# Performance work log

Hardware: AMD Instinct MI355X
Metric: run time of the kernel (lower is better)

Reference implementation:

```python
import jax, jax.numpy as jnp
import numpy as np

N, E, NNZ, F = 65536, 16384, 786432, 128
ALPHA, BETA = 0.5, 0.5


def _linear(x, w, b):
    # torch nn.Linear: x @ W^T + b, W is [out,in]
    return x @ w.T + b


def _spmm_to_edges(vals, node_idx, hedge_idx, m):
    # (sparse [E,N]) @ m[N,F] -> [E,F]
    return jax.ops.segment_sum(vals[:, None] * m[node_idx], hedge_idx, num_segments=E)


def _spmm_to_nodes(vals, node_idx, hedge_idx, m):
    # (sparse [N,E]) @ m[E,F] -> [N,F]
    return jax.ops.segment_sum(vals[:, None] * m[hedge_idx], node_idx, num_segments=N)


def setup_inputs() -> dict:
    key = jax.random.key(0)
    ks = jax.random.split(key, 16)
    stdv = 1.0 / np.sqrt(F)
    u = lambda k, shp: jax.random.uniform(k, shp, jnp.float32, -stdv, stdv)
    return {
        "x": jax.random.normal(ks[0], (N, F), jnp.float32),
        "y": jax.random.normal(ks[1], (E, F), jnp.float32),
        "node_idx": jax.random.randint(ks[2], (NNZ,), 0, N, jnp.int32),
        "hedge_idx": jax.random.randint(ks[3], (NNZ,), 0, E, jnp.int32),
        "hd_vals": jax.random.uniform(ks[4], (NNZ,), jnp.float32),
        "hb_vals": jax.random.uniform(ks[5], (NNZ,), jnp.float32),
        "dhwd_vals": jax.random.uniform(ks[6], (NNZ,), jnp.float32),
        "bhub_vals": jax.random.uniform(ks[7], (NNZ,), jnp.float32),
        "Qv_w": u(ks[8], (F, F)), "Qv_b": u(ks[9], (F,)),
        "Qe_w": u(ks[10], (F, F)), "Qe_b": u(ks[11], (F,)),
        "Pe_w": u(ks[12], (F, F)), "Pe_b": u(ks[13], (F,)),
        "Pv_w": u(ks[14], (F, F)), "Pv_b": u(ks[15], (F,)),
    }


def reference(x, y, node_idx, hedge_idx, hd_vals, hb_vals, dhwd_vals, bhub_vals,
              Qv_w, Qv_b, Qe_w, Qe_b, Pe_w, Pe_b, Pv_w, Pv_b):
    qvx = _linear(x, Qv_w, Qv_b)          # [N,F]
    qey = _linear(y, Qe_w, Qe_b)          # [E,F]
    pey = _linear(y, Pe_w, Pe_b)          # [E,F]
    pvx = _linear(x, Pv_w, Pv_b)          # [N,F]
    # X = DHWD @ (alpha * (HD @ Qv(x)) + (1-alpha) * Qe(y))
    t_e = ALPHA * _spmm_to_edges(hd_vals, node_idx, hedge_idx, qvx) + (1.0 - ALPHA) * qey
    X = _spmm_to_nodes(dhwd_vals, node_idx, hedge_idx, t_e)
    # Y = BHUB @ (beta * (HB @ Pe(y)) + (1-beta) * Pv(x))
    t_n = BETA * _spmm_to_nodes(hb_vals, node_idx, hedge_idx, pey) + (1.0 - BETA) * pvx
    Y = _spmm_to_edges(bhub_vals, node_idx, hedge_idx, t_n)
    return (X, Y)
```

## Files before the change

kernel.cpp:

```cpp
#include <hip/hip_runtime.h>

#define F 128
#define NN 65536
#define EE 16384
#define NNZT 786432

typedef __attribute__((ext_vector_type(8))) short bfrag8;
typedef __attribute__((ext_vector_type(4))) float f32x4;

__device__ __forceinline__ unsigned int bfrn(float f) {
    unsigned int u = __float_as_uint(f);
    return (u + 0x7fffu + ((u >> 16) & 1u)) >> 16;
}

__global__ void hist_kernel(const int4* __restrict__ hedge_idx4,
                            const int4* __restrict__ node_idx4,
                            int* __restrict__ cnt_e, int* __restrict__ cnt_n) {
    int i = blockIdx.x * 256 + threadIdx.x;
    int4 e = hedge_idx4[i];
    int4 n = node_idx4[i];
    atomicAdd(&cnt_e[e.x], 1);
    atomicAdd(&cnt_e[e.y], 1);
    atomicAdd(&cnt_e[e.z], 1);
    atomicAdd(&cnt_e[e.w], 1);
    atomicAdd(&cnt_n[n.x], 1);
    atomicAdd(&cnt_n[n.y], 1);
    atomicAdd(&cnt_n[n.z], 1);
    atomicAdd(&cnt_n[n.w], 1);
}

__global__ __launch_bounds__(1024) void scan_p1(const int* __restrict__ cnt,
                                                int* __restrict__ ofs,
                                                int* __restrict__ bsum) {
    __shared__ int wsum[16];
    int t = threadIdx.x, lane = t & 63, w = t >> 6;
    int g = blockIdx.x * 1024 + t;
    int v = cnt[g];
    int inc = v;
#pragma unroll
    for (int d = 1; d < 64; d <<= 1) {
        int u = __shfl_up(inc, d);
        if (lane >= d) inc += u;
    }
    if (lane == 63) wsum[w] = inc;
    __syncthreads();
    if (t < 16) {
        int s = wsum[t];
#pragma unroll
        for (int d = 1; d < 16; d <<= 1) {
            int u = __shfl_up(s, d);
            if (t >= d) s += u;
        }
        wsum[t] = s;
    }
    __syncthreads();
    int woff = (w == 0) ? 0 : wsum[w - 1];
    ofs[g] = woff + inc - v;
    if (t == 1023) bsum[blockIdx.x] = wsum[15];
}

__global__ void scan_p2(int* __restrict__ bsum, int nb, int* __restrict__ ofs_end) {
    int lane = threadIdx.x;
    int v = (lane < nb) ? bsum[lane] : 0;
    int inc = v;
#pragma unroll
    for (int d = 1; d < 64; d <<= 1) {
        int u = __shfl_up(inc, d);
        if (lane >= d) inc += u;
    }
    if (lane < nb) bsum[lane] = inc - v;
    if (lane == 63) *ofs_end = inc;
}

__global__ __launch_bounds__(1024) void scan_p3(int* __restrict__ ofs,
                                                const int* __restrict__ bsum) {
    int g = blockIdx.x * 1024 + threadIdx.x;
    ofs[g] += bsum[blockIdx.x];
}

__global__ void fill_kernel(const int* __restrict__ node_idx, const int* __restrict__ hedge_idx,
                            const float* __restrict__ hd_vals, const float* __restrict__ hb_vals,
                            const float* __restrict__ dhwd_vals, const float* __restrict__ bhub_vals,
                            const int* __restrict__ ofs_e, const int* __restrict__ ofs_n,
                            int* __restrict__ cur_e, int* __restrict__ cur_n,
                            int* __restrict__ csr_e_node, float* __restrict__ csr_e_v1, float* __restrict__ csr_e_v2,
                            int* __restrict__ csr_n_edge, float* __restrict__ csr_n_v1, float* __restrict__ csr_n_v2) {
    int i = blockIdx.x * 256 + threadIdx.x;
    int e = hedge_idx[i];
    int n = node_idx[i];
    int pe = atomicAdd(&cur_e[e], 1);
    int oe = ofs_e[e] + pe;
    csr_e_node[oe] = n;
    csr_e_v1[oe] = 0.5f * hd_vals[i];
    csr_e_v2[oe] = bhub_vals[i];
    int pn = atomicAdd(&cur_n[n], 1);
    int on = ofs_n[n] + pn;
    csr_n_edge[on] = e;
    csr_n_v1[on] = 0.5f * hb_vals[i];
    csr_n_v2[on] = dhwd_vals[i];
}

__global__ void wprep_kernel(const float* __restrict__ W0, const float* __restrict__ W1,
                             const float* __restrict__ W2, const float* __restrict__ W3,
                             unsigned short* __restrict__ whi, unsigned short* __restrict__ wlo) {
    int mat = blockIdx.x >> 6;
    int off = (blockIdx.x & 63) * 256 + threadIdx.x;
    const float* W = (mat == 0) ? W0 : (mat == 1) ? W1 : (mat == 2) ? W2 : W3;
    float f = W[off];
    unsigned int h = bfrn(f);
    float hf = __uint_as_float(h << 16);
    unsigned int l = bfrn(f - hf);
    int idx = mat * 16384 + off;
    whi[idx] = (unsigned short)h;
    wlo[idx] = (unsigned short)l;
}

__global__ __launch_bounds__(256, 2) void gemm_mfma(const float* __restrict__ in,
                                                    const unsigned short* __restrict__ whi,
                                                    const unsigned short* __restrict__ wlo,
                                                    const float* __restrict__ bA,
                                                    const float* __restrict__ bB,
                                                    float* __restrict__ outA,
                                                    float* __restrict__ outB) {
    __shared__ uint4 AH[2][4][64];
    __shared__ uint4 AL[2][4][64];
    int t = threadIdx.x;
    int wv = t >> 6, lane = t & 63;
    int row0 = blockIdx.x * 128;

    int mat = wv >> 1;
    const unsigned short* wh = whi + mat * 16384;
    const unsigned short* wl = wlo + mat * 16384;
    int colbase = (wv & 1) * 64;
    int ln15 = lane & 15;
    int kb = 8 * (lane >> 4);

    bfrag8 bh[4][4], bl[4][4];
#pragma unroll
    for (int ct = 0; ct < 4; ++ct) {
        int n = colbase + ct * 16 + ln15;
#pragma unroll
        for (int ks = 0; ks < 4; ++ks) {
            bh[ct][ks] = *(const bfrag8*)&wh[n * 128 + ks * 32 + kb];
            bl[ct][ks] = *(const bfrag8*)&wl[n * 128 + ks * 32 + kb];
        }
    }
    const float* bias = mat ? bB : bA;
    float biasv[4];
#pragma unroll
    for (int ct = 0; ct < 4; ++ct) biasv[ct] = bias[colbase + ct * 16 + ln15];
    float* outp = mat ? outB : outA;

    auto STAGE = [&](int rt, int b) {
        int r = row0 + rt * 16 + ln15;
        int k0 = wv * 32 + kb;
        const float* p = &in[(size_t)r * 128 + k0];
        float4 f0 = *(const float4*)p;
        float4 f1 = *(const float4*)(p + 4);
        float fs[8] = {f0.x, f0.y, f0.z, f0.w, f1.x, f1.y, f1.z, f1.w};
        unsigned int hi[4], lo[4];
#pragma unroll
        for (int q = 0; q < 4; ++q) {
            unsigned int h0 = bfrn(fs[2 * q]);
            unsigned int h1 = bfrn(fs[2 * q + 1]);
            float hf0 = __uint_as_float(h0 << 16);
            float hf1 = __uint_as_float(h1 << 16);
            unsigned int l0 = bfrn(fs[2 * q] - hf0);
            unsigned int l1 = bfrn(fs[2 * q + 1] - hf1);
            hi[q] = h0 | (h1 << 16);
            lo[q] = l0 | (l1 << 16);
        }
        AH[b][wv][lane] = make_uint4(hi[0], hi[1], hi[2], hi[3]);
        AL[b][wv][lane] = make_uint4(lo[0], lo[1], lo[2], lo[3]);
    };

    STAGE(0, 0);
    __syncthreads();
    for (int rt = 0; rt < 8; ++rt) {
        int b = rt & 1;
        if (rt < 7) STAGE(rt + 1, b ^ 1);
        f32x4 acc[4];
#pragma unroll
        for (int ct = 0; ct < 4; ++ct) acc[ct] = (f32x4){0.f, 0.f, 0.f, 0.f};
#pragma unroll
        for (int ks = 0; ks < 4; ++ks) {
            bfrag8 ah = *(const bfrag8*)&AH[b][ks][lane];
            bfrag8 al = *(const bfrag8*)&AL[b][ks][lane];
#pragma unroll
            for (int ct = 0; ct < 4; ++ct)
                acc[ct] = __builtin_amdgcn_mfma_f32_16x16x32_bf16(ah, bh[ct][ks], acc[ct], 0, 0, 0);
#pragma unroll
            for (int ct = 0; ct < 4; ++ct)
                acc[ct] = __builtin_amdgcn_mfma_f32_16x16x32_bf16(ah, bl[ct][ks], acc[ct], 0, 0, 0);
#pragma unroll
            for (int ct = 0; ct < 4; ++ct)
                acc[ct] = __builtin_amdgcn_mfma_f32_16x16x32_bf16(al, bh[ct][ks], acc[ct], 0, 0, 0);
        }
        int rbase = row0 + rt * 16 + (lane >> 4) * 4;
#pragma unroll
        for (int ct = 0; ct < 4; ++ct) {
            int c = colbase + ct * 16 + ln15;
#pragma unroll
            for (int rg = 0; rg < 4; ++rg)
                outp[(size_t)(rbase + rg) * 128 + c] = acc[ct][rg] + biasv[ct];
        }
        __syncthreads();
    }
}

template <int U, bool NT>
__global__ __launch_bounds__(256) void spmm_gather4(const int* __restrict__ ofs,
                                                    const int* __restrict__ tgt,
                                                    const float* __restrict__ val,
                                                    const float* __restrict__ src,
                                                    float* __restrict__ out,
                                                    float init_scale) {
    int row = blockIdx.x * 4 + (threadIdx.x >> 6);
    int lane = threadIdx.x & 63;
    int half = lane >> 5;
    int li = lane & 31;
    int o0 = ofs[row], o1 = ofs[row + 1];
    float4 acc = {0.f, 0.f, 0.f, 0.f};
    int j = o0;
    for (; j + 2 * U - 1 < o1; j += 2 * U) {
        int tg[U];
        float v[U];
#pragma unroll
        for (int u = 0; u < U; ++u) {
            tg[u] = tgt[j + 2 * u + half];
            v[u] = val[j + 2 * u + half];
        }
        float4 m[U];
#pragma unroll
        for (int u = 0; u < U; ++u) m[u] = *(const float4*)&src[(size_t)tg[u] * F + li * 4];
#pragma unroll
        for (int u = 0; u < U; ++u) {
            acc.x += v[u] * m[u].x;
            acc.y += v[u] * m[u].y;
            acc.z += v[u] * m[u].z;
            acc.w += v[u] * m[u].w;
        }
    }
    for (; j < o1; j += 2) {
        int idx = j + half;
        bool ok = idx < o1;
        int tg = ok ? tgt[idx] : tgt[o0];
        float v = ok ? val[idx] : 0.f;
        float4 m = *(const float4*)&src[(size_t)tg * F + li * 4];
        acc.x += v * m.x;
        acc.y += v * m.y;
        acc.z += v * m.z;
        acc.w += v * m.w;
    }
    acc.x += __shfl_down(acc.x, 32);
    acc.y += __shfl_down(acc.y, 32);
    acc.z += __shfl_down(acc.z, 32);
    acc.w += __shfl_down(acc.w, 32);
    if (half == 0) {
        float4* op = (float4*)&out[(size_t)row * F + li * 4];
        if (init_scale != 0.0f) {
            float4 in0 = *op;
            acc.x += init_scale * in0.x;
            acc.y += init_scale * in0.y;
            acc.z += init_scale * in0.z;
            acc.w += init_scale * in0.w;
        }
        if (NT) {
            __builtin_nontemporal_store(*(f32x4*)&acc, (f32x4*)op);
        } else {
            *op = acc;
        }
    }
}

extern "C" void kernel_launch(void* const* d_in, const int* in_sizes, int n_in,
                              void* d_out, int out_size, void* d_ws, size_t ws_size,
                              hipStream_t stream) {
    const float* x = (const float*)d_in[0];
    const float* y = (const float*)d_in[1];
    const int* node_idx = (const int*)d_in[2];
    const int* hedge_idx = (const int*)d_in[3];
    const float* hd_vals = (const float*)d_in[4];
    const float* hb_vals = (const float*)d_in[5];
    const float* dhwd_vals = (const float*)d_in[6];
    const float* bhub_vals = (const float*)d_in[7];
    const float* Qv_w = (const float*)d_in[8];
    const float* Qv_b = (const float*)d_in[9];
    const float* Qe_w = (const float*)d_in[10];
    const float* Qe_b = (const float*)d_in[11];
    const float* Pe_w = (const float*)d_in[12];
    const float* Pe_b = (const float*)d_in[13];
    const float* Pv_w = (const float*)d_in[14];
    const float* Pv_b = (const float*)d_in[15];

    float* X = (float*)d_out;
    float* Y = (float*)d_out + (size_t)NN * F;
    float* qvx = X;
    float* pey = Y;

    char* w = (char*)d_ws;
    float* t_n        = (float*)(w + 0);
    float* t_e        = (float*)(w + 33554432);
    int*   csr_e_node = (int*)  (w + 41943040);
    float* csr_e_v1   = (float*)(w + 45088768);
    float* csr_e_v2   = (float*)(w + 48234496);
    int*   csr_n_edge = (int*)  (w + 51380224);
    float* csr_n_v1   = (float*)(w + 54525952);
    float* csr_n_v2   = (float*)(w + 57671680);
    int*   cnt_e      = (int*)  (w + 60817408);
    int*   cnt_n      = (int*)  (w + 60882944);
    int*   cur_e      = (int*)  (w + 61145088);
    int*   cur_n      = (int*)  (w + 61210624);
    int*   ofs_e      = (int*)  (w + 61472768);
    int*   ofs_n      = (int*)  (w + 61538560);
    int*   bsum       = (int*)  (w + 61800960);
    unsigned short* whi = (unsigned short*)(w + 60882944);
    unsigned short* wlo = (unsigned short*)(w + 60882944 + 131072);

    (void)hipMemsetAsync(cnt_e, 0, (size_t)2 * (EE + NN) * 4, stream);

    hist_kernel<<<NNZT / 1024, 256, 0, stream>>>((const int4*)hedge_idx, (const int4*)node_idx,
                                                 cnt_e, cnt_n);

    scan_p1<<<EE / 1024, 1024, 0, stream>>>(cnt_e, ofs_e, bsum);
    scan_p2<<<1, 64, 0, stream>>>(bsum, EE / 1024, &ofs_e[EE]);
    scan_p3<<<EE / 1024, 1024, 0, stream>>>(ofs_e, bsum);
    scan_p1<<<NN / 1024, 1024, 0, stream>>>(cnt_n, ofs_n, bsum);
    scan_p2<<<1, 64, 0, stream>>>(bsum, NN / 1024, &ofs_n[NN]);
    scan_p3<<<NN / 1024, 1024, 0, stream>>>(ofs_n, bsum);

    fill_kernel<<<NNZT / 256, 256, 0, stream>>>(node_idx, hedge_idx, hd_vals, hb_vals,
                                                dhwd_vals, bhub_vals, ofs_e, ofs_n,
                                                cur_e, cur_n,
                                                csr_e_node, csr_e_v1, csr_e_v2,
                                                csr_n_edge, csr_n_v1, csr_n_v2);

    wprep_kernel<<<256, 256, 0, stream>>>(Qv_w, Pv_w, Qe_w, Pe_w, whi, wlo);

    gemm_mfma<<<NN / 128, 256, 0, stream>>>(x, whi, wlo, Qv_b, Pv_b, qvx, t_n);
    gemm_mfma<<<EE / 128, 256, 0, stream>>>(y, whi + 2 * 16384, wlo + 2 * 16384,
                                            Qe_b, Pe_b, t_e, pey);

    spmm_gather4<4, false><<<EE / 4, 256, 0, stream>>>(ofs_e, csr_e_node, csr_e_v1, qvx, t_e, 0.5f);
    spmm_gather4<4, false><<<NN / 4, 256, 0, stream>>>(ofs_n, csr_n_edge, csr_n_v1, pey, t_n, 0.5f);

    spmm_gather4<4, true><<<NN / 4, 256, 0, stream>>>(ofs_n, csr_n_edge, csr_n_v2, t_e, X, 0.0f);
    spmm_gather4<4, true><<<EE / 4, 256, 0, stream>>>(ofs_e, csr_e_node, csr_e_v2, t_n, Y, 0.0f);
}
```

Baseline: 555.9 us.

## Store gathered intermediates in bf16 and replace CSR value copies with inverse permutation

The GEMM outputs and the intermediate t_e/t_n that get gathered by the SpMMs are now stored as bf16, which halves the bytes of each random row gather. The fill kernel now writes only an inverse permutation instead of copying indices and four value arrays into CSR order. The SpMMs look up the index and value through that permutation, and each quarter-wave gathers 16-byte bf16 row chunks. This trades numerical precision in the intermediates (bf16 rounding) and an extra level of indirect loads for less fill-kernel traffic and less gather bandwidth.

```diff
diff --git a/kernel.cpp b/kernel.cpp
--- a/kernel.cpp
+++ b/kernel.cpp
@@ -78,26 +78,17 @@
     ofs[g] += bsum[blockIdx.x];
 }
 
-__global__ void fill_kernel(const int* __restrict__ node_idx, const int* __restrict__ hedge_idx,
-                            const float* __restrict__ hd_vals, const float* __restrict__ hb_vals,
-                            const float* __restrict__ dhwd_vals, const float* __restrict__ bhub_vals,
-                            const int* __restrict__ ofs_e, const int* __restrict__ ofs_n,
-                            int* __restrict__ cur_e, int* __restrict__ cur_n,
-                            int* __restrict__ csr_e_node, float* __restrict__ csr_e_v1, float* __restrict__ csr_e_v2,
-                            int* __restrict__ csr_n_edge, float* __restrict__ csr_n_v1, float* __restrict__ csr_n_v2) {
+__global__ void invfill_kernel(const int* __restrict__ node_idx, const int* __restrict__ hedge_idx,
+                               const int* __restrict__ ofs_e, const int* __restrict__ ofs_n,
+                               int* __restrict__ cur_e, int* __restrict__ cur_n,
+                               int* __restrict__ inv_e, int* __restrict__ inv_n) {
     int i = blockIdx.x * 256 + threadIdx.x;
     int e = hedge_idx[i];
+    int pe = atomicAdd(&cur_e[e], 1);
+    inv_e[ofs_e[e] + pe] = i;
     int n = node_idx[i];
-    int pe = atomicAdd(&cur_e[e], 1);
-    int oe = ofs_e[e] + pe;
-    csr_e_node[oe] = n;
-    csr_e_v1[oe] = 0.5f * hd_vals[i];
-    csr_e_v2[oe] = bhub_vals[i];
     int pn = atomicAdd(&cur_n[n], 1);
-    int on = ofs_n[n] + pn;
-    csr_n_edge[on] = e;
-    csr_n_v1[on] = 0.5f * hb_vals[i];
-    csr_n_v2[on] = dhwd_vals[i];
+    inv_n[ofs_n[n] + pn] = i;
 }
 
 __global__ void wprep_kernel(const float* __restrict__ W0, const float* __restrict__ W1,
@@ -115,13 +106,14 @@
     wlo[idx] = (unsigned short)l;
 }
 
+template <bool ABF16, bool BBF16>
 __global__ __launch_bounds__(256, 2) void gemm_mfma(const float* __restrict__ in,
                                                     const unsigned short* __restrict__ whi,
                                                     const unsigned short* __restrict__ wlo,
                                                     const float* __restrict__ bA,
                                                     const float* __restrict__ bB,
-                                                    float* __restrict__ outA,
-                                                    float* __restrict__ outB) {
+                                                    void* __restrict__ outA,
+                                                    void* __restrict__ outB) {
     __shared__ uint4 AH[2][4][64];
     __shared__ uint4 AL[2][4][64];
     int t = threadIdx.x;
@@ -149,7 +141,8 @@
     float biasv[4];
 #pragma unroll
     for (int ct = 0; ct < 4; ++ct) biasv[ct] = bias[colbase + ct * 16 + ln15];
-    float* outp = mat ? outB : outA;
+    void* outp = mat ? outB : outA;
+    bool obf = mat ? BBF16 : ABF16;
 
     auto STAGE = [&](int rt, int b) {
         int r = row0 + rt * 16 + ln15;
@@ -201,74 +194,87 @@
         for (int ct = 0; ct < 4; ++ct) {
             int c = colbase + ct * 16 + ln15;
 #pragma unroll
-            for (int rg = 0; rg < 4; ++rg)
-                outp[(size_t)(rbase + rg) * 128 + c] = acc[ct][rg] + biasv[ct];
+            for (int rg = 0; rg < 4; ++rg) {
+                float v = acc[ct][rg] + biasv[ct];
+                if (obf)
+                    ((unsigned short*)outp)[(size_t)(rbase + rg) * 128 + c] = (unsigned short)bfrn(v);
+                else
+                    ((float*)outp)[(size_t)(rbase + rg) * 128 + c] = v;
+            }
         }
         __syncthreads();
     }
 }
 
-template <int U, bool NT>
-__global__ __launch_bounds__(256) void spmm_gather4(const int* __restrict__ ofs,
-                                                    const int* __restrict__ tgt,
-                                                    const float* __restrict__ val,
-                                                    const float* __restrict__ src,
-                                                    float* __restrict__ out,
-                                                    float init_scale) {
+template <int U, bool BF16OUT, bool HASINIT>
+__global__ __launch_bounds__(256) void spmm_g(const int* __restrict__ ofs,
+                                              const int* __restrict__ inv,
+                                              const int* __restrict__ idxarr,
+                                              const float* __restrict__ valarr,
+                                              float vscale,
+                                              const unsigned short* __restrict__ src,
+                                              const float* __restrict__ initsrc,
+                                              float iscale,
+                                              void* __restrict__ outp) {
     int row = blockIdx.x * 4 + (threadIdx.x >> 6);
     int lane = threadIdx.x & 63;
-    int half = lane >> 5;
-    int li = lane & 31;
+    int q = lane >> 4;
+    int li = lane & 15;
     int o0 = ofs[row], o1 = ofs[row + 1];
-    float4 acc = {0.f, 0.f, 0.f, 0.f};
-    int j = o0;
-    for (; j + 2 * U - 1 < o1; j += 2 * U) {
-        int tg[U];
-        float v[U];
+    float acc[8] = {};
+    for (int j = o0; j < o1; j += 4 * U) {
 #pragma unroll
         for (int u = 0; u < U; ++u) {
-            tg[u] = tgt[j + 2 * u + half];
-            v[u] = val[j + 2 * u + half];
-        }
-        float4 m[U];
-#pragma unroll
-        for (int u = 0; u < U; ++u) m[u] = *(const float4*)&src[(size_t)tg[u] * F + li * 4];
-#pragma unroll
-        for (int u = 0; u < U; ++u) {
-            acc.x += v[u] * m[u].x;
-            acc.y += v[u] * m[u].y;
-            acc.z += v[u] * m[u].z;
-            acc.w += v[u] * m[u].w;
-        }
-    }
-    for (; j < o1; j += 2) {
-        int idx = j + half;
-        bool ok = idx < o1;
-        int tg = ok ? tgt[idx] : tgt[o0];
-        float v = ok ? val[idx] : 0.f;
-        float4 m = *(const float4*)&src[(size_t)tg * F + li * 4];
-        acc.x += v * m.x;
-        acc.y += v * m.y;
-        acc.z += v * m.z;
-        acc.w += v * m.w;
-    }
-    acc.x += __shfl_down(acc.x, 32);
-    acc.y += __shfl_down(acc.y, 32);
-    acc.z += __shfl_down(acc.z, 32);
-    acc.w += __shfl_down(acc.w, 32);
-    if (half == 0) {
-        float4* op = (float4*)&out[(size_t)row * F + li * 4];
-        if (init_scale != 0.0f) {
-            float4 in0 = *op;
-            acc.x += init_scale * in0.x;
-            acc.y += init_scale * in0.y;
-            acc.z += init_scale * in0.z;
-            acc.w += init_scale * in0.w;
-        }
-        if (NT) {
-            __builtin_nontemporal_store(*(f32x4*)&acc, (f32x4*)op);
+            int slot = j + 4 * u + q;
+            bool ok = slot < o1;
+            int ss = ok ? slot : o0;
+            int iv = inv[ss];
+            int tg = idxarr[iv];
+            float v = ok ? valarr[iv] * vscale : 0.f;
+            uint4 rb = *(const uint4*)&src[(size_t)tg * F + li * 8];
+            unsigned int rw0 = rb.x, rw1 = rb.y, rw2 = rb.z, rw3 = rb.w;
+            acc[0] += v * __uint_as_float(rw0 << 16);
+            acc[1] += v * __uint_as_float(rw0 & 0xffff0000u);
+            acc[2] += v * __uint_as_float(rw1 << 16);
+            acc[3] += v * __uint_as_float(rw1 & 0xffff0000u);
+            acc[4] += v * __uint_as_float(rw2 << 16);
+            acc[5] += v * __uint_as_float(rw2 & 0xffff0000u);
+            acc[6] += v * __uint_as_float(rw3 << 16);
+            acc[7] += v * __uint_as_float(rw3 & 0xffff0000u);
+        }
+    }
+#pragma unroll
+    for (int k = 0; k < 8; ++k) {
+        acc[k] += __shfl_down(acc[k], 32);
+        acc[k] += __shfl_down(acc[k], 16);
+    }
+    if (q == 0) {
+        if (HASINIT) {
+            const float4* ip = (const float4*)&initsrc[(size_t)row * F + li * 8];
+            float4 i0 = ip[0], i1 = ip[1];
+            acc[0] += iscale * i0.x;
+            acc[1] += iscale * i0.y;
+            acc[2] += iscale * i0.z;
+            acc[3] += iscale * i0.w;
+            acc[4] += iscale * i1.x;
+            acc[5] += iscale * i1.y;
+            acc[6] += iscale * i1.z;
+            acc[7] += iscale * i1.w;
+        }
+        if (BF16OUT) {
+            unsigned short* ob = (unsigned short*)outp;
+            uint4 wv;
+            wv.x = bfrn(acc[0]) | (bfrn(acc[1]) << 16);
+            wv.y = bfrn(acc[2]) | (bfrn(acc[3]) << 16);
+            wv.z = bfrn(acc[4]) | (bfrn(acc[5]) << 16);
+            wv.w = bfrn(acc[6]) | (bfrn(acc[7]) << 16);
+            *(uint4*)&ob[(size_t)row * F + li * 8] = wv;
         } else {
-            *op = acc;
+            float* of = (float*)outp;
+            float4 s0 = {acc[0], acc[1], acc[2], acc[3]};
+            float4 s1 = {acc[4], acc[5], acc[6], acc[7]};
+            *(float4*)&of[(size_t)row * F + li * 8] = s0;
+            *(float4*)&of[(size_t)row * F + li * 8 + 4] = s1;
         }
     }
 }
@@ -295,27 +301,25 @@
 
     float* X = (float*)d_out;
     float* Y = (float*)d_out + (size_t)NN * F;
-    float* qvx = X;
-    float* pey = Y;
+    float* pvx = X;
+    float* qey = Y;
 
     char* w = (char*)d_ws;
-    float* t_n        = (float*)(w + 0);
-    float* t_e        = (float*)(w + 33554432);
-    int*   csr_e_node = (int*)  (w + 41943040);
-    float* csr_e_v1   = (float*)(w + 45088768);
-    float* csr_e_v2   = (float*)(w + 48234496);
-    int*   csr_n_edge = (int*)  (w + 51380224);
-    float* csr_n_v1   = (float*)(w + 54525952);
-    float* csr_n_v2   = (float*)(w + 57671680);
-    int*   cnt_e      = (int*)  (w + 60817408);
-    int*   cnt_n      = (int*)  (w + 60882944);
-    int*   cur_e      = (int*)  (w + 61145088);
-    int*   cur_n      = (int*)  (w + 61210624);
-    int*   ofs_e      = (int*)  (w + 61472768);
-    int*   ofs_n      = (int*)  (w + 61538560);
-    int*   bsum       = (int*)  (w + 61800960);
-    unsigned short* whi = (unsigned short*)(w + 60882944);
-    unsigned short* wlo = (unsigned short*)(w + 60882944 + 131072);
+    unsigned short* qvx_b = (unsigned short*)(w + 0);
+    unsigned short* pey_b = (unsigned short*)(w + 16777216);
+    unsigned short* t_e_b = (unsigned short*)(w + 20971520);
+    unsigned short* t_n_b = (unsigned short*)(w + 25165824);
+    int* inv_e = (int*)(w + 41943040);
+    int* inv_n = (int*)(w + 45088768);
+    int* cnt_e = (int*)(w + 48234496);
+    int* cnt_n = (int*)(w + 48300032);
+    int* cur_e = (int*)(w + 48562176);
+    int* cur_n = (int*)(w + 48627712);
+    int* ofs_e = (int*)(w + 48889856);
+    int* ofs_n = (int*)(w + 48956416);
+    int* bsum  = (int*)(w + 49219072);
+    unsigned short* whi = (unsigned short*)(w + 49219328);
+    unsigned short* wlo = (unsigned short*)(w + 49350400);
 
     (void)hipMemsetAsync(cnt_e, 0, (size_t)2 * (EE + NN) * 4, stream);
 
@@ -329,21 +333,22 @@
     scan_p2<<<1, 64, 0, stream>>>(bsum, NN / 1024, &ofs_n[NN]);
     scan_p3<<<NN / 1024, 1024, 0, stream>>>(ofs_n, bsum);
 
-    fill_kernel<<<NNZT / 256, 256, 0, stream>>>(node_idx, hedge_idx, hd_vals, hb_vals,
-                                                dhwd_vals, bhub_vals, ofs_e, ofs_n,
-                                                cur_e, cur_n,
-                                                csr_e_node, csr_e_v1, csr_e_v2,
-                                                csr_n_edge, csr_n_v1, csr_n_v2);
+    invfill_kernel<<<NNZT / 256, 256, 0, stream>>>(node_idx, hedge_idx, ofs_e, ofs_n,
+                                                   cur_e, cur_n, inv_e, inv_n);
 
     wprep_kernel<<<256, 256, 0, stream>>>(Qv_w, Pv_w, Qe_w, Pe_w, whi, wlo);
 
-    gemm_mfma<<<NN / 128, 256, 0, stream>>>(x, whi, wlo, Qv_b, Pv_b, qvx, t_n);
-    gemm_mfma<<<EE / 128, 256, 0, stream>>>(y, whi + 2 * 16384, wlo + 2 * 16384,
-                                            Qe_b, Pe_b, t_e, pey);
-
-    spmm_gather4<4, false><<<EE / 4, 256, 0, stream>>>(ofs_e, csr_e_node, csr_e_v1, qvx, t_e, 0.5f);
-    spmm_gather4<4, false><<<NN / 4, 256, 0, stream>>>(ofs_n, csr_n_edge, csr_n_v1, pey, t_n, 0.5f);
-
-    spmm_gather4<4, true><<<NN / 4, 256, 0, stream>>>(ofs_n, csr_n_edge, csr_n_v2, t_e, X, 0.0f);
-    spmm_gather4<4, true><<<EE / 4, 256, 0, stream>>>(ofs_e, csr_e_node, csr_e_v2, t_n, Y, 0.0f);
-}
+    gemm_mfma<true, false><<<NN / 128, 256, 0, stream>>>(x, whi, wlo, Qv_b, Pv_b, qvx_b, pvx);
+    gemm_mfma<false, true><<<EE / 128, 256, 0, stream>>>(y, whi + 2 * 16384, wlo + 2 * 16384,
+                                                         Qe_b, Pe_b, qey, pey_b);
+
+    spmm_g<4, true, true><<<EE / 4, 256, 0, stream>>>(ofs_e, inv_e, node_idx, hd_vals, 0.5f,
+                                                      qvx_b, qey, 0.5f, t_e_b);
+    spmm_g<2, true, true><<<NN / 4, 256, 0, stream>>>(ofs_n, inv_n, hedge_idx, hb_vals, 0.5f,
+                                                      pey_b, pvx, 0.5f, t_n_b);
+
+    spmm_g<2, false, false><<<NN / 4, 256, 0, stream>>>(ofs_n, inv_n, hedge_idx, dhwd_vals, 1.0f,
+                                                        t_e_b, nullptr, 0.f, X);
+    spmm_g<4, false, false><<<EE / 4, 256, 0, stream>>>(ofs_e, inv_e, node_idx, bhub_vals, 1.0f,
+                                                        t_n_b, nullptr, 0.f, Y);
+}
```

Measured after the change: 515.6 us. 1.08x faster.
